# Optimization experiments

Measured on AMD Instinct MI355X. Metric: run time of the kernel, lower is better.

## Reference

```python
import jax, jax.numpy as jnp
import numpy as np

EPS = 1e-06


def _bilinear_sample(feat, coords_norm):
    """torch F.grid_sample(mode='bilinear', padding_mode='border', align_corners=False).
    feat: [B,C,H,W], coords_norm: [B,N,2] with (x,y) in [-1,1]. Returns [B,N,C]."""
    B, C, H, W = feat.shape
    # unnormalize (align_corners=False), then border-clip the coordinate
    x = jnp.clip(((coords_norm[..., 0] + 1.0) * W - 1.0) * 0.5, 0.0, W - 1.0)
    y = jnp.clip(((coords_norm[..., 1] + 1.0) * H - 1.0) * 0.5, 0.0, H - 1.0)
    x0 = jnp.floor(x); y0 = jnp.floor(y)
    wx = (x - x0)[:, None, :]; wy = (y - y0)[:, None, :]  # [B,1,N]
    x0i = x0.astype(jnp.int32); y0i = y0.astype(jnp.int32)
    x1i = jnp.minimum(x0i + 1, W - 1); y1i = jnp.minimum(y0i + 1, H - 1)
    flat = feat.reshape(B, C, H * W)
    def gather(yi, xi):
        idx = yi * W + xi  # [B,N]
        return jnp.take_along_axis(flat, idx[:, None, :], axis=2)  # [B,C,N]
    v00 = gather(y0i, x0i); v01 = gather(y0i, x1i)
    v10 = gather(y1i, x0i); v11 = gather(y1i, x1i)
    out = (v00 * (1 - wx) * (1 - wy) + v01 * wx * (1 - wy)
           + v10 * (1 - wx) * wy + v11 * wx * wy)
    return out.transpose(0, 2, 1)  # [B,N,C]


def _lin(x, w, b):
    return x @ w + b


def _forward(img, feat_s8, feat1_s8, feat_s16, ctx_s8, coarse_flow,
             ctx_w, ctx_b, gate1, ffn1_w1, ffn1_b1, ffn1_w2, ffn1_b2,
             s8_w, s8_b, gate2, ffn2_w1, ffn2_b1, ffn2_w2, ffn2_b2,
             hw1, hb1, hw2, hb2, hw3, hb3, hw4, hb4):
    B, _, H8, W8 = feat_s8.shape
    Hf, Wf = H8 * 8, W8 * 8
    # dense query grid in full-res pixel coords
    xs = jnp.arange(Wf, dtype=jnp.float32)
    ys = jnp.arange(Hf, dtype=jnp.float32)
    gx, gy = jnp.meshgrid(xs, ys)  # each [Hf,Wf]
    cn_x = jnp.clip(2.0 * (gx.reshape(-1) + 0.5) / Wf - 1.0, -1 + EPS, 1 - EPS)
    cn_y = jnp.clip(2.0 * (gy.reshape(-1) + 0.5) / Hf - 1.0, -1 + EPS, 1 - EPS)
    coords_norm = jnp.broadcast_to(jnp.stack([cn_x, cn_y], -1)[None], (B, Hf * Wf, 2))
    # five bilinear lookups
    f16 = _bilinear_sample(feat_s16, coords_norm)
    f8 = _bilinear_sample(feat_s8, coords_norm)
    fctx = _bilinear_sample(ctx_s8, coords_norm)
    # gated FFN fusion
    h2 = f8 + jax.nn.sigmoid(gate1) * _lin(fctx, ctx_w, ctx_b)
    h2 = _lin(jax.nn.gelu(_lin(h2, ffn1_w1, ffn1_b1), approximate=False), ffn1_w2, ffn1_b2)
    h3 = f16 + jax.nn.sigmoid(gate2) * _lin(h2, s8_w, s8_b)
    fused = _lin(jax.nn.gelu(_lin(h3, ffn2_w1, ffn2_b1), approximate=False), ffn2_w2, ffn2_b2)
    # coarse flow at queries, scaled to full-res pixels (Wf/W8 = Hf/H8 = 8)
    coarse = _bilinear_sample(coarse_flow, coords_norm) * jnp.array([Wf / W8, Hf / H8], jnp.float32)
    warp_x = coords_norm[..., 0] + 2.0 * coarse[..., 0] / Wf
    warp_y = coords_norm[..., 1] + 2.0 * coarse[..., 1] / Hf
    warped = jnp.clip(jnp.stack([warp_x, warp_y], -1), -1 + EPS, 1 - EPS)
    f1w = _bilinear_sample(feat1_s8, warped)
    coarse_norm = coarse / jnp.array([Wf, Hf], jnp.float32)
    mlp_in = jnp.concatenate([fused, f1w, coords_norm, coarse_norm], axis=-1)  # [B,N,260]
    h = jax.nn.relu(_lin(mlp_in, hw1, hb1))
    h = jax.nn.relu(_lin(h, hw2, hb2))
    h = jax.nn.relu(_lin(h, hw3, hb3))
    delta_norm = _lin(h, hw4, hb4)  # [B,N,2]
    flow = coarse + delta_norm * jnp.array([Wf, Hf], jnp.float32)
    return flow.reshape(B, Hf, Wf, 2).transpose(0, 3, 1, 2)


def setup_inputs() -> dict:
    key = jax.random.key(0)
    ks = jax.random.split(key, 24)
    hd = 128
    d = {
        'img': jax.random.normal(ks[0], (2, 3, 384, 512), jnp.float32),
        'feat_s8': jax.random.normal(ks[1], (2, 128, 48, 64), jnp.float32),
        'feat1_s8': jax.random.normal(ks[2], (2, 128, 48, 64), jnp.float32),
        'feat_s16': jax.random.normal(ks[3], (2, 128, 24, 32), jnp.float32),
        'ctx_s8': jax.random.normal(ks[4], (2, 64, 48, 64), jnp.float32),
        'coarse_flow': jax.random.normal(ks[5], (2, 2, 48, 64), jnp.float32),
        'ctx_w': jax.random.normal(ks[6], (64, hd), jnp.float32) * 0.05,
        'ctx_b': jnp.zeros((hd,), jnp.float32),
        'gate1': jnp.ones((hd,), jnp.float32),
        'ffn1_w1': jax.random.normal(ks[7], (hd, 2 * hd), jnp.float32) * 0.05,
        'ffn1_b1': jnp.zeros((2 * hd,), jnp.float32),
        'ffn1_w2': jax.random.normal(ks[8], (2 * hd, hd), jnp.float32) * 0.05,
        'ffn1_b2': jnp.zeros((hd,), jnp.float32),
        's8_w': jax.random.normal(ks[9], (hd, hd), jnp.float32) * 0.05,
        's8_b': jnp.zeros((hd,), jnp.float32),
        'gate2': jnp.ones((hd,), jnp.float32),
        'ffn2_w1': jax.random.normal(ks[10], (hd, 2 * hd), jnp.float32) * 0.05,
        'ffn2_b1': jnp.zeros((2 * hd,), jnp.float32),
        'ffn2_w2': jax.random.normal(ks[11], (2 * hd, hd), jnp.float32) * 0.05,
        'ffn2_b2': jnp.zeros((hd,), jnp.float32),
        'hw1': jax.random.normal(ks[12], (hd + 128 + 2 + 2, 256), jnp.float32) * 0.05,
        'hb1': jnp.zeros((256,), jnp.float32),
        'hw2': jax.random.normal(ks[13], (256, 128), jnp.float32) * 0.05,
        'hb2': jnp.zeros((128,), jnp.float32),
        'hw3': jax.random.normal(ks[14], (128, 64), jnp.float32) * 0.05,
        'hb3': jnp.zeros((64,), jnp.float32),
        'hw4': jax.random.normal(ks[15], (64, 2), jnp.float32) * 0.05,
        'hb4': jnp.zeros((2,), jnp.float32),
    }
    return d


def reference(img, feat_s8, feat1_s8, feat_s16, ctx_s8, coarse_flow,
              ctx_w, ctx_b, gate1, ffn1_w1, ffn1_b1, ffn1_w2, ffn1_b2,
              s8_w, s8_b, gate2, ffn2_w1, ffn2_b1, ffn2_w2, ffn2_b2,
              hw1, hb1, hw2, hb2, hw3, hb3, hw4, hb4):
    return _forward(img, feat_s8, feat1_s8, feat_s16, ctx_s8, coarse_flow,
                    ctx_w, ctx_b, gate1, ffn1_w1, ffn1_b1, ffn1_w2, ffn1_b2,
                    s8_w, s8_b, gate2, ffn2_w1, ffn2_b1, ffn2_w2, ffn2_b2,
                    hw1, hb1, hw2, hb2, hw3, hb3, hw4, hb4)
```

## Files before the change

### kernel.cpp

```cpp
#include <hip/hip_runtime.h>
#include <math.h>


typedef _Float16 half8 __attribute__((ext_vector_type(8)));
typedef _Float16 half4v __attribute__((ext_vector_type(4)));
typedef _Float16 half2v __attribute__((ext_vector_type(2)));
typedef float floatx4 __attribute__((ext_vector_type(4)));

#define NPOINTS_TOTAL (2 * 384 * 512)
#define PPB 64
#define NBLOCKS (NPOINTS_TOTAL / PPB)
#define PTS_PER_IMG 196608
#define BLOCKS_PER_IMG 3072

#define WS_CTX   0
#define WS_F1W1  8192
#define WS_F1W2  40960
#define WS_S8    73728
#define WS_F2W1  90112
#define WS_F2W2  122880
#define WS_HW1   155648
#define WS_HW2   221184
#define WS_HW3   253952

#define SB_CTXB  0
#define SB_GATE1 128
#define SB_F1B1  256
#define SB_F1B2  512
#define SB_S8B   640
#define SB_GATE2 768
#define SB_F2B1  896
#define SB_F2B2  1152
#define SB_HB1   1280
#define SB_HB2   1536
#define SB_HB3   1664
#define SB_TOT   1728

__device__ __forceinline__ float sigmoidf_(float x) { return 1.0f / (1.0f + expf(-x)); }
__device__ __forceinline__ float geluf_(float x) {
    const float ax = fabsf(x) * 0.70710678118654752f;
    const float t = 1.0f / fmaf(0.3275911f, ax, 1.0f);
    float poly = fmaf(t, 1.061405429f, -1.453152027f);
    poly = fmaf(t, poly, 1.421413741f);
    poly = fmaf(t, poly, -0.284496736f);
    poly = fmaf(t, poly, 0.254829592f);
    poly *= t;
    float er = 1.0f - poly * expf(-ax * ax);
    er = copysignf(er, x);
    return 0.5f * x * (1.0f + er);
}
__device__ __forceinline__ int swz(int pt) { return (pt & 15) << 3; }

__global__ void prepack_kernel(const float* __restrict__ ctx_w, const float* __restrict__ f1w1,
                               const float* __restrict__ f1w2, const float* __restrict__ s8w,
                               const float* __restrict__ f2w1, const float* __restrict__ f2w2,
                               const float* __restrict__ hw1, const float* __restrict__ hw2,
                               const float* __restrict__ hw3, _Float16* __restrict__ ws) {
    const int bid = blockIdx.x;
    const int lane = threadIdx.x;
    const float* src; int N, CT, start; size_t ofsH;
    if (bid < 16)       { src = ctx_w; N = 128; CT = 8;  start = 0;   ofsH = WS_CTX; }
    else if (bid < 80)  { src = f1w1;  N = 256; CT = 16; start = 16;  ofsH = WS_F1W1; }
    else if (bid < 144) { src = f1w2;  N = 128; CT = 8;  start = 80;  ofsH = WS_F1W2; }
    else if (bid < 176) { src = s8w;   N = 128; CT = 8;  start = 144; ofsH = WS_S8; }
    else if (bid < 240) { src = f2w1;  N = 256; CT = 16; start = 176; ofsH = WS_F2W1; }
    else if (bid < 304) { src = f2w2;  N = 128; CT = 8;  start = 240; ofsH = WS_F2W2; }
    else if (bid < 432) { src = hw1;   N = 256; CT = 16; start = 304; ofsH = WS_HW1; }
    else if (bid < 496) { src = hw2;   N = 128; CT = 8;  start = 432; ofsH = WS_HW2; }
    else                { src = hw3;   N = 64;  CT = 4;  start = 496; ofsH = WS_HW3; }
    const int ti = bid - start;
    const int ks = ti / CT, ct = ti % CT;
    const int m = lane & 15, g = lane >> 4;
    const int kb = ks * 32 + g * 8;
    const int n = ct * 16 + m;
    half8 v;
#pragma unroll
    for (int j = 0; j < 8; ++j) v[j] = (_Float16)src[(size_t)(kb + j) * N + n];
    *reinterpret_cast<half8*>(ws + ofsH + (size_t)ti * 512 + lane * 8) = v;
}

template <int NT, int CTc>
__device__ __forceinline__ void stageChunk(const _Float16* __restrict__ src, int cts,
                                           int ks0, int ct0, _Float16* wdst,
                                           int wid, int lane) {
#pragma unroll
    for (int jj = 0; jj < NT / 4; ++jj) {
        const int j = wid * (NT / 4) + jj;
        const int ks = j / CTc, ct = j - ks * CTc;
        const _Float16* s = src + (((size_t)(ks0 + ks) * cts + (ct0 + ct)) << 9) + lane * 8;
        _Float16* d = wdst + ((size_t)j << 9);
        __builtin_amdgcn_global_load_lds(
            (const __attribute__((address_space(1))) unsigned int*)s,
            (__attribute__((address_space(3))) unsigned int*)d, 16, 0, 0);
    }
}

template <int KSc, int CT>
__device__ __forceinline__ void gemmChunk(floatx4 (&acc)[CT], const _Float16* wlds,
                                          const _Float16* sact, int kbase, int ptb, int lane) {
    const int m = lane & 15, g = lane >> 4;
    const int pt0 = ptb + m;
    const int s0 = swz(pt0);
    const _Float16* wb = wlds + lane * 8;
    __builtin_amdgcn_s_setprio(1);
#pragma unroll
    for (int ks = 0; ks < KSc; ++ks) {
        half8 a = *reinterpret_cast<const half8*>(
            sact + pt0 * 128 + ((((kbase + ks) * 32) + g * 8) ^ s0));
        const _Float16* wk = wb + ((size_t)(ks * CT) << 9);
#pragma unroll
        for (int ct = 0; ct < CT; ++ct) {
            half8 w = *reinterpret_cast<const half8*>(wk + ((size_t)ct << 9));
            acc[ct] = __builtin_amdgcn_mfma_f32_16x16x32_f16(w, a, acc[ct], 0, 0, 0);
        }
    }
    __builtin_amdgcn_s_setprio(0);
}

template <int KSc, int CT>
__device__ __forceinline__ void gemmChunkRegB(floatx4 (&acc)[CT], const _Float16* wlds,
                                              const half8 (&fr)[4], int frbase, int lane) {
    const _Float16* wb = wlds + lane * 8;
    __builtin_amdgcn_s_setprio(1);
#pragma unroll
    for (int ks = 0; ks < KSc; ++ks) {
        const _Float16* wk = wb + ((size_t)(ks * CT) << 9);
#pragma unroll
        for (int ct = 0; ct < CT; ++ct) {
            half8 w = *reinterpret_cast<const half8*>(wk + ((size_t)ct << 9));
            acc[ct] = __builtin_amdgcn_mfma_f32_16x16x32_f16(w, fr[frbase + ks], acc[ct], 0, 0, 0);
        }
    }
    __builtin_amdgcn_s_setprio(0);
}

__device__ __forceinline__ void loadFrags(half8 (&fr)[4], const _Float16* sact, int ptb, int lane) {
    const int m = lane & 15, g = lane >> 4;
    const int pt0 = ptb + m;
    const int s0 = swz(pt0);
#pragma unroll
    for (int ks = 0; ks < 4; ++ks)
        fr[ks] = *reinterpret_cast<const half8*>(sact + pt0 * 128 + ((ks * 32 + g * 8) ^ s0));
}

__device__ __forceinline__ void storeH4(_Float16* dst, int pt, int ch0,
                                        float o0, float o1, float o2, float o3) {
    half4v hv;
    hv[0] = (_Float16)o0; hv[1] = (_Float16)o1; hv[2] = (_Float16)o2; hv[3] = (_Float16)o3;
    *reinterpret_cast<half4v*>(dst + pt * 128 + (ch0 ^ swz(pt))) = hv;
}
__device__ __forceinline__ half4v loadH4(const _Float16* src, int pt, int ch0) {
    return *reinterpret_cast<const half4v*>(src + pt * 128 + (ch0 ^ swz(pt)));
}

__global__ void __launch_bounds__(256, 2)
ifd_mfma(const float* __restrict__ feat_s8, const float* __restrict__ feat1_s8,
         const float* __restrict__ feat_s16, const float* __restrict__ ctx_s8,
         const float* __restrict__ coarse_flow,
         const float* __restrict__ ctx_b, const float* __restrict__ gate1,
         const float* __restrict__ ffn1_b1, const float* __restrict__ ffn1_b2,
         const float* __restrict__ s8_b, const float* __restrict__ gate2,
         const float* __restrict__ ffn2_b1, const float* __restrict__ ffn2_b2,
         const float* __restrict__ hw1, const float* __restrict__ hb1,
         const float* __restrict__ hb2, const float* __restrict__ hb3,
         const float* __restrict__ hw4, const float* __restrict__ hb4,
         const _Float16* __restrict__ wsp, float* __restrict__ out) {
    __shared__ __align__(16) _Float16 bufA[64 * 128];
    __shared__ __align__(16) _Float16 bufB[64 * 128];
    __shared__ __align__(16) _Float16 wBuf[2][8192];
    __shared__ __align__(16) float sBias[SB_TOT];
    __shared__ float sScal[4 * 64];
    __shared__ float sCps[2 * 64];
    __shared__ int   sIdx[3 * 4 * 64];
    __shared__ float sWgt[3 * 2 * 64];

    const int t = threadIdx.x;
    const int lane = t & 63, wid = t >> 6;
    const int m = lane & 15, g = lane >> 4;
    const int ptb = wid * 16;
    const int b = blockIdx.x / BLOCKS_PER_IMG;
    const int qbase = blockIdx.x * PPB;
    const float CHI = 1.0f - 1e-6f;

    if (t < 128) {
        sBias[SB_CTXB + t] = ctx_b[t];
        sBias[SB_GATE1 + t] = gate1[t];
        sBias[SB_F1B2 + t] = ffn1_b2[t];
        sBias[SB_S8B + t] = s8_b[t];
        sBias[SB_GATE2 + t] = gate2[t];
        sBias[SB_F2B2 + t] = ffn2_b2[t];
        sBias[SB_HB2 + t] = hb2[t];
    }
    sBias[SB_F1B1 + t] = ffn1_b1[t];
    sBias[SB_F2B1 + t] = ffn2_b1[t];
    sBias[SB_HB1 + t] = hb1[t];
    if (t < 64) sBias[SB_HB3 + t] = hb3[t];

    if (t < 64) {
        const int p = t;
        const int rem = qbase + p - b * PTS_PER_IMG;
        const int gy = rem >> 9, gx = rem & 511;
        float cnx = fminf(fmaxf(2.0f * ((float)gx + 0.5f) / 512.0f - 1.0f, -CHI), CHI);
        float cny = fminf(fmaxf(2.0f * ((float)gy + 0.5f) / 384.0f - 1.0f, -CHI), CHI);

        auto mkc = [](float cn, float Sf, int Smax, int& i0, int& i1, float& w) {
            float x = fminf(fmaxf(((cn + 1.0f) * Sf - 1.0f) * 0.5f, 0.0f), Sf - 1.0f);
            float xf = floorf(x);
            w = x - xf;
            i0 = (int)xf;
            i1 = (i0 + 1 > Smax) ? Smax : i0 + 1;
        };
        auto storeSet = [&](int s, int x0, int x1, int y0, int y1, float wx, float wy) {
            sIdx[s * 256 + 0 * 64 + p] = x0; sIdx[s * 256 + 1 * 64 + p] = x1;
            sIdx[s * 256 + 2 * 64 + p] = y0; sIdx[s * 256 + 3 * 64 + p] = y1;
            sWgt[s * 128 + p] = wx; sWgt[s * 128 + 64 + p] = wy;
        };

        int x0, x1, y0, y1; float wx, wy;
        mkc(cnx, 64.0f, 63, x0, x1, wx);
        mkc(cny, 48.0f, 47, y0, y1, wy);
        storeSet(0, x0, x1, y0, y1, wx, wy);

        int X0, X1, Y0, Y1; float WX, WY;
        mkc(cnx, 32.0f, 31, X0, X1, WX);
        mkc(cny, 24.0f, 23, Y0, Y1, WY);
        storeSet(1, X0, X1, Y0, Y1, WX, WY);

        const float w00 = (1.0f - wx) * (1.0f - wy), w01 = wx * (1.0f - wy);
        const float w10 = (1.0f - wx) * wy, w11 = wx * wy;
        const int i00 = y0 * 64 + x0, i01 = y0 * 64 + x1, i10 = y1 * 64 + x0, i11 = y1 * 64 + x1;
        const float* cf = coarse_flow + (size_t)b * 6144;
        float c0 = (cf[i00] * w00 + cf[i01] * w01 + cf[i10] * w10 + cf[i11] * w11) * 8.0f;
        const float* cf1 = cf + 3072;
        float c1 = (cf1[i00] * w00 + cf1[i01] * w01 + cf1[i10] * w10 + cf1[i11] * w11) * 8.0f;
        sCps[p] = c0; sCps[64 + p] = c1;
        sScal[p] = cnx; sScal[64 + p] = cny;
        sScal[128 + p] = c0 / 512.0f; sScal[192 + p] = c1 / 384.0f;

        float wxn = fminf(fmaxf(cnx + 2.0f * c0 / 512.0f, -CHI), CHI);
        float wyn = fminf(fmaxf(cny + 2.0f * c1 / 384.0f, -CHI), CHI);
        int u0, u1, v0, v1; float uw, vw;
        mkc(wxn, 64.0f, 63, u0, u1, uw);
        mkc(wyn, 48.0f, 47, v0, v1, vw);
        storeSet(2, u0, u1, v0, v1, uw, vw);
    }

    stageChunk<16, 8>(wsp + WS_CTX, 8, 0, 0, wBuf[0], wid, lane);
    __syncthreads();

    auto sampleMap = [&](const float* __restrict__ mapB, int C, int HW, int Wd, int set,
                         _Float16* dst) {
        const int pt = t & 63, hs = t >> 6;
        const int x0 = sIdx[set * 256 + pt], x1 = sIdx[set * 256 + 64 + pt];
        const int y0 = sIdx[set * 256 + 128 + pt], y1 = sIdx[set * 256 + 192 + pt];
        const float wx = sWgt[set * 128 + pt], wy = sWgt[set * 128 + 64 + pt];
        const float w00 = (1.0f - wx) * (1.0f - wy), w01 = wx * (1.0f - wy);
        const float w10 = (1.0f - wx) * wy, w11 = wx * wy;
        const int i00 = y0 * Wd + x0, i01 = y0 * Wd + x1, i10 = y1 * Wd + x0, i11 = y1 * Wd + x1;
        const int np = C >> 3;
#pragma unroll 4
        for (int i = 0; i < np; ++i) {
            const int c0 = hs * (C >> 2) + 2 * i;
            const float* p0 = mapB + (size_t)c0 * HW;
            const float* p1 = p0 + HW;
            float v0 = p0[i00] * w00 + p0[i01] * w01 + p0[i10] * w10 + p0[i11] * w11;
            float v1 = p1[i00] * w00 + p1[i01] * w01 + p1[i10] * w10 + p1[i11] * w11;
            half2v hv; hv[0] = (_Float16)v0; hv[1] = (_Float16)v1;
            *reinterpret_cast<half2v*>(dst + pt * 128 + (c0 ^ swz(pt))) = hv;
        }
    };

    sampleMap(feat_s8 + (size_t)b * 128 * 3072, 128, 3072, 64, 0, bufA);
    sampleMap(ctx_s8 + (size_t)b * 64 * 3072, 64, 3072, 64, 0, bufB);
    __syncthreads();

    const int pt = ptb + m;
    int cur = 0;
    floatx4 acc[8];

#define RESET8() do { _Pragma("unroll") for (int c = 0; c < 8; ++c) acc[c] = (floatx4)0.0f; } while (0)
#define STEP_END() do { __syncthreads(); cur ^= 1; } while (0)

    stageChunk<16, 8>(wsp + WS_F1W1, 16, 0, 0, wBuf[cur ^ 1], wid, lane);
    RESET8();
    gemmChunk<2, 8>(acc, wBuf[cur], bufB, 0, ptb, lane);
#pragma unroll
    for (int ct = 0; ct < 8; ++ct) {
        const int ch0 = ct * 16 + g * 4;
        const float4 bb = *reinterpret_cast<const float4*>(sBias + SB_CTXB + ch0);
        const float4 gg = *reinterpret_cast<const float4*>(sBias + SB_GATE1 + ch0);
        half4v rv = loadH4(bufA, pt, ch0);
        floatx4 v = acc[ct];
        storeH4(bufA, pt, ch0,
                (float)rv[0] + sigmoidf_(gg.x) * (v[0] + bb.x),
                (float)rv[1] + sigmoidf_(gg.y) * (v[1] + bb.y),
                (float)rv[2] + sigmoidf_(gg.z) * (v[2] + bb.z),
                (float)rv[3] + sigmoidf_(gg.w) * (v[3] + bb.w));
    }
    STEP_END();

    stageChunk<16, 8>(wsp + WS_F1W1, 16, 2, 0, wBuf[cur ^ 1], wid, lane);
    RESET8();
    gemmChunk<2, 8>(acc, wBuf[cur], bufA, 0, ptb, lane);
    STEP_END();
    stageChunk<16, 8>(wsp + WS_F1W1, 16, 0, 8, wBuf[cur ^ 1], wid, lane);
    gemmChunk<2, 8>(acc, wBuf[cur], bufA, 2, ptb, lane);
#pragma unroll
    for (int ct = 0; ct < 8; ++ct) {
        const int ch0 = ct * 16 + g * 4;
        const float4 bb = *reinterpret_cast<const float4*>(sBias + SB_F1B1 + ch0);
        floatx4 v = acc[ct];
        storeH4(bufB, pt, ch0, geluf_(v[0] + bb.x), geluf_(v[1] + bb.y),
                geluf_(v[2] + bb.z), geluf_(v[3] + bb.w));
    }
    STEP_END();

    stageChunk<16, 8>(wsp + WS_F1W1, 16, 2, 8, wBuf[cur ^ 1], wid, lane);
    RESET8();
    gemmChunk<2, 8>(acc, wBuf[cur], bufA, 0, ptb, lane);
    STEP_END();
    stageChunk<16, 8>(wsp + WS_F1W2, 8, 0, 0, wBuf[cur ^ 1], wid, lane);
    gemmChunk<2, 8>(acc, wBuf[cur], bufA, 2, ptb, lane);
#pragma unroll
    for (int ct = 0; ct < 8; ++ct) {
        const int ch0 = ct * 16 + g * 4;
        const float4 bb = *reinterpret_cast<const float4*>(sBias + SB_F1B1 + 128 + ch0);
        floatx4 v = acc[ct];
        storeH4(bufA, pt, ch0, geluf_(v[0] + bb.x), geluf_(v[1] + bb.y),
                geluf_(v[2] + bb.z), geluf_(v[3] + bb.w));
    }
    STEP_END();

    stageChunk<16, 8>(wsp + WS_F1W2, 8, 2, 0, wBuf[cur ^ 1], wid, lane);
    RESET8();
    gemmChunk<2, 8>(acc, wBuf[cur], bufB, 0, ptb, lane);
    STEP_END();
    stageChunk<16, 8>(wsp + WS_F1W2, 8, 4, 0, wBuf[cur ^ 1], wid, lane);
    gemmChunk<2, 8>(acc, wBuf[cur], bufB, 2, ptb, lane);
    STEP_END();
    stageChunk<16, 8>(wsp + WS_F1W2, 8, 6, 0, wBuf[cur ^ 1], wid, lane);
    gemmChunk<2, 8>(acc, wBuf[cur], bufA, 0, ptb, lane);
    STEP_END();
    stageChunk<16, 8>(wsp + WS_S8, 8, 0, 0, wBuf[cur ^ 1], wid, lane);
    gemmChunk<2, 8>(acc, wBuf[cur], bufA, 2, ptb, lane);
#pragma unroll
    for (int ct = 0; ct < 8; ++ct) {
        const int ch0 = ct * 16 + g * 4;
        const float4 bb = *reinterpret_cast<const float4*>(sBias + SB_F1B2 + ch0);
        floatx4 v = acc[ct];
        storeH4(bufA, pt, ch0, v[0] + bb.x, v[1] + bb.y, v[2] + bb.z, v[3] + bb.w);
    }
    STEP_END();

    sampleMap(feat_s16 + (size_t)b * 128 * 768, 128, 768, 32, 1, bufB);
    __syncthreads();

    stageChunk<16, 8>(wsp + WS_S8, 8, 2, 0, wBuf[cur ^ 1], wid, lane);
    RESET8();
    gemmChunk<2, 8>(acc, wBuf[cur], bufA, 0, ptb, lane);
    STEP_END();
    stageChunk<16, 8>(wsp + WS_F2W1, 16, 0, 0, wBuf[cur ^ 1], wid, lane);
    gemmChunk<2, 8>(acc, wBuf[cur], bufA, 2, ptb, lane);
#pragma unroll
    for (int ct = 0; ct < 8; ++ct) {
        const int ch0 = ct * 16 + g * 4;
        const float4 bb = *reinterpret_cast<const float4*>(sBias + SB_S8B + ch0);
        const float4 gg = *reinterpret_cast<const float4*>(sBias + SB_GATE2 + ch0);
        half4v rv = loadH4(bufB, pt, ch0);
        floatx4 v = acc[ct];
        storeH4(bufB, pt, ch0,
                (float)rv[0] + sigmoidf_(gg.x) * (v[0] + bb.x),
                (float)rv[1] + sigmoidf_(gg.y) * (v[1] + bb.y),
                (float)rv[2] + sigmoidf_(gg.z) * (v[2] + bb.z),
                (float)rv[3] + sigmoidf_(gg.w) * (v[3] + bb.w));
    }
    STEP_END();

    stageChunk<16, 8>(wsp + WS_F2W1, 16, 2, 0, wBuf[cur ^ 1], wid, lane);
    RESET8();
    gemmChunk<2, 8>(acc, wBuf[cur], bufB, 0, ptb, lane);
    STEP_END();
    stageChunk<16, 8>(wsp + WS_F2W1, 16, 0, 8, wBuf[cur ^ 1], wid, lane);
    gemmChunk<2, 8>(acc, wBuf[cur], bufB, 2, ptb, lane);
#pragma unroll
    for (int ct = 0; ct < 8; ++ct) {
        const int ch0 = ct * 16 + g * 4;
        const float4 bb = *reinterpret_cast<const float4*>(sBias + SB_F2B1 + ch0);
        floatx4 v = acc[ct];
        storeH4(bufA, pt, ch0, geluf_(v[0] + bb.x), geluf_(v[1] + bb.y),
                geluf_(v[2] + bb.z), geluf_(v[3] + bb.w));
    }
    STEP_END();

    stageChunk<16, 8>(wsp + WS_F2W1, 16, 2, 8, wBuf[cur ^ 1], wid, lane);
    RESET8();
    gemmChunk<2, 8>(acc, wBuf[cur], bufB, 0, ptb, lane);
    STEP_END();
    stageChunk<16, 8>(wsp + WS_F2W2, 8, 0, 0, wBuf[cur ^ 1], wid, lane);
    gemmChunk<2, 8>(acc, wBuf[cur], bufB, 2, ptb, lane);
#pragma unroll
    for (int ct = 0; ct < 8; ++ct) {
        const int ch0 = ct * 16 + g * 4;
        const float4 bb = *reinterpret_cast<const float4*>(sBias + SB_F2B1 + 128 + ch0);
        floatx4 v = acc[ct];
        storeH4(bufB, pt, ch0, geluf_(v[0] + bb.x), geluf_(v[1] + bb.y),
                geluf_(v[2] + bb.z), geluf_(v[3] + bb.w));
    }
    STEP_END();

    stageChunk<16, 8>(wsp + WS_F2W2, 8, 2, 0, wBuf[cur ^ 1], wid, lane);
    RESET8();
    gemmChunk<2, 8>(acc, wBuf[cur], bufA, 0, ptb, lane);
    STEP_END();
    stageChunk<16, 8>(wsp + WS_F2W2, 8, 4, 0, wBuf[cur ^ 1], wid, lane);
    gemmChunk<2, 8>(acc, wBuf[cur], bufA, 2, ptb, lane);
    STEP_END();
    stageChunk<16, 8>(wsp + WS_F2W2, 8, 6, 0, wBuf[cur ^ 1], wid, lane);
    gemmChunk<2, 8>(acc, wBuf[cur], bufB, 0, ptb, lane);
    STEP_END();
    stageChunk<16, 8>(wsp + WS_HW1, 16, 0, 0, wBuf[cur ^ 1], wid, lane);
    gemmChunk<2, 8>(acc, wBuf[cur], bufB, 2, ptb, lane);
#pragma unroll
    for (int ct = 0; ct < 8; ++ct) {
        const int ch0 = ct * 16 + g * 4;
        const float4 bb = *reinterpret_cast<const float4*>(sBias + SB_F2B2 + ch0);
        floatx4 v = acc[ct];
        storeH4(bufB, pt, ch0, v[0] + bb.x, v[1] + bb.y, v[2] + bb.z, v[3] + bb.w);
    }
    STEP_END();

    sampleMap(feat1_s8 + (size_t)b * 128 * 3072, 128, 3072, 64, 2, bufA);
    __syncthreads();

    half8 fr[4];
    loadFrags(fr, bufA, ptb, lane);
    stageChunk<16, 8>(wsp + WS_HW1, 16, 2, 0, wBuf[cur ^ 1], wid, lane);
    RESET8();
    gemmChunk<2, 8>(acc, wBuf[cur], bufB, 0, ptb, lane);
    STEP_END();
    stageChunk<16, 8>(wsp + WS_HW1, 16, 4, 0, wBuf[cur ^ 1], wid, lane);
    gemmChunk<2, 8>(acc, wBuf[cur], bufB, 2, ptb, lane);
    STEP_END();
    stageChunk<16, 8>(wsp + WS_HW1, 16, 6, 0, wBuf[cur ^ 1], wid, lane);
    gemmChunkRegB<2, 8>(acc, wBuf[cur], fr, 0, lane);
    STEP_END();
    stageChunk<16, 8>(wsp + WS_HW1, 16, 0, 8, wBuf[cur ^ 1], wid, lane);
    gemmChunkRegB<2, 8>(acc, wBuf[cur], fr, 2, lane);
#pragma unroll
    for (int ct = 0; ct < 8; ++ct) {
        const int ch0 = ct * 16 + g * 4;
#pragma unroll
        for (int jj = 0; jj < 4; ++jj) {
            const float4 wj = *reinterpret_cast<const float4*>(hw1 + (size_t)(256 + jj) * 256 + ch0);
            const float s = sScal[jj * 64 + pt];
            floatx4 v = acc[ct];
            v[0] = fmaf(wj.x, s, v[0]); v[1] = fmaf(wj.y, s, v[1]);
            v[2] = fmaf(wj.z, s, v[2]); v[3] = fmaf(wj.w, s, v[3]);
            acc[ct] = v;
        }
        const float4 bb = *reinterpret_cast<const float4*>(sBias + SB_HB1 + ch0);
        floatx4 v = acc[ct];
        storeH4(bufA, pt, ch0, fmaxf(v[0] + bb.x, 0.0f), fmaxf(v[1] + bb.y, 0.0f),
                fmaxf(v[2] + bb.z, 0.0f), fmaxf(v[3] + bb.w, 0.0f));
    }
    STEP_END();

    stageChunk<16, 8>(wsp + WS_HW1, 16, 2, 8, wBuf[cur ^ 1], wid, lane);
    RESET8();
    gemmChunk<2, 8>(acc, wBuf[cur], bufB, 0, ptb, lane);
    STEP_END();
    stageChunk<16, 8>(wsp + WS_HW1, 16, 4, 8, wBuf[cur ^ 1], wid, lane);
    gemmChunk<2, 8>(acc, wBuf[cur], bufB, 2, ptb, lane);
    STEP_END();
    stageChunk<16, 8>(wsp + WS_HW1, 16, 6, 8, wBuf[cur ^ 1], wid, lane);
    gemmChunkRegB<2, 8>(acc, wBuf[cur], fr, 0, lane);
    STEP_END();
    stageChunk<16, 8>(wsp + WS_HW2, 8, 0, 0, wBuf[cur ^ 1], wid, lane);
    gemmChunkRegB<2, 8>(acc, wBuf[cur], fr, 2, lane);
#pragma unroll
    for (int ct = 0; ct < 8; ++ct) {
        const int ch0 = ct * 16 + g * 4;
#pragma unroll
        for (int jj = 0; jj < 4; ++jj) {
            const float4 wj = *reinterpret_cast<const float4*>(hw1 + (size_t)(256 + jj) * 256 + 128 + ch0);
            const float s = sScal[jj * 64 + pt];
            floatx4 v = acc[ct];
            v[0] = fmaf(wj.x, s, v[0]); v[1] = fmaf(wj.y, s, v[1]);
            v[2] = fmaf(wj.z, s, v[2]); v[3] = fmaf(wj.w, s, v[3]);
            acc[ct] = v;
        }
        const float4 bb = *reinterpret_cast<const float4*>(sBias + SB_HB1 + 128 + ch0);
        floatx4 v = acc[ct];
        storeH4(bufB, pt, ch0, fmaxf(v[0] + bb.x, 0.0f), fmaxf(v[1] + bb.y, 0.0f),
                fmaxf(v[2] + bb.z, 0.0f), fmaxf(v[3] + bb.w, 0.0f));
    }
    STEP_END();

    stageChunk<16, 8>(wsp + WS_HW2, 8, 2, 0, wBuf[cur ^ 1], wid, lane);
    RESET8();
    gemmChunk<2, 8>(acc, wBuf[cur], bufA, 0, ptb, lane);
    STEP_END();
    stageChunk<16, 8>(wsp + WS_HW2, 8, 4, 0, wBuf[cur ^ 1], wid, lane);
    gemmChunk<2, 8>(acc, wBuf[cur], bufA, 2, ptb, lane);
    STEP_END();
    stageChunk<16, 8>(wsp + WS_HW2, 8, 6, 0, wBuf[cur ^ 1], wid, lane);
    gemmChunk<2, 8>(acc, wBuf[cur], bufB, 0, ptb, lane);
    STEP_END();
    stageChunk<16, 4>(wsp + WS_HW3, 4, 0, 0, wBuf[cur ^ 1], wid, lane);
    gemmChunk<2, 8>(acc, wBuf[cur], bufB, 2, ptb, lane);
#pragma unroll
    for (int ct = 0; ct < 8; ++ct) {
        const int ch0 = ct * 16 + g * 4;
        const float4 bb = *reinterpret_cast<const float4*>(sBias + SB_HB2 + ch0);
        floatx4 v = acc[ct];
        storeH4(bufA, pt, ch0, fmaxf(v[0] + bb.x, 0.0f), fmaxf(v[1] + bb.y, 0.0f),
                fmaxf(v[2] + bb.z, 0.0f), fmaxf(v[3] + bb.w, 0.0f));
    }
    STEP_END();

    {
        floatx4 acc4[4];
#pragma unroll
        for (int c = 0; c < 4; ++c) acc4[c] = (floatx4)0.0f;
        gemmChunk<4, 4>(acc4, wBuf[cur], bufA, 0, ptb, lane);
#pragma unroll
        for (int ct = 0; ct < 4; ++ct) {
            const int ch0 = ct * 16 + g * 4;
            const float4 bb = *reinterpret_cast<const float4*>(sBias + SB_HB3 + ch0);
            floatx4 v = acc4[ct];
            storeH4(bufB, pt, ch0, fmaxf(v[0] + bb.x, 0.0f), fmaxf(v[1] + bb.y, 0.0f),
                    fmaxf(v[2] + bb.z, 0.0f), fmaxf(v[3] + bb.w, 0.0f));
        }
    }
    __syncthreads();

    if (t < 128) {
        const int pp = t >> 1, j = t & 1;
        float d = hb4[j];
#pragma unroll
        for (int i8 = 0; i8 < 8; ++i8) {
            const int c0 = i8 * 8;
            half8 hv = *reinterpret_cast<const half8*>(bufB + pp * 128 + (c0 ^ swz(pp)));
#pragma unroll
            for (int j2 = 0; j2 < 8; ++j2)
                d = fmaf((float)hv[j2], hw4[(c0 + j2) * 2 + j], d);
        }
        const int q = qbase + pp;
        const int rem = q - b * PTS_PER_IMG;
        const int gy = rem >> 9, gx = rem & 511;
        const float flow = sCps[j * 64 + pp] + d * (j == 0 ? 512.0f : 384.0f);
        out[(((size_t)b * 2 + j) * 384 + gy) * 512 + gx] = flow;
    }
#undef RESET8
#undef STEP_END
}

extern "C" void kernel_launch(void* const* d_in, const int* in_sizes, int n_in,
                              void* d_out, int out_size, void* d_ws, size_t ws_size,
                              hipStream_t stream) {
    const float* feat_s8 = (const float*)d_in[1];
    const float* feat1_s8 = (const float*)d_in[2];
    const float* feat_s16 = (const float*)d_in[3];
    const float* ctx_s8 = (const float*)d_in[4];
    const float* coarse_flow = (const float*)d_in[5];
    const float* ctx_w = (const float*)d_in[6];
    const float* ctx_b = (const float*)d_in[7];
    const float* gate1 = (const float*)d_in[8];
    const float* ffn1_w1 = (const float*)d_in[9];
    const float* ffn1_b1 = (const float*)d_in[10];
    const float* ffn1_w2 = (const float*)d_in[11];
    const float* ffn1_b2 = (const float*)d_in[12];
    const float* s8_w = (const float*)d_in[13];
    const float* s8_b = (const float*)d_in[14];
    const float* gate2 = (const float*)d_in[15];
    const float* ffn2_w1 = (const float*)d_in[16];
    const float* ffn2_b1 = (const float*)d_in[17];
    const float* ffn2_w2 = (const float*)d_in[18];
    const float* ffn2_b2 = (const float*)d_in[19];
    const float* hw1 = (const float*)d_in[20];
    const float* hb1 = (const float*)d_in[21];
    const float* hw2 = (const float*)d_in[22];
    const float* hb2 = (const float*)d_in[23];
    const float* hw3 = (const float*)d_in[24];
    const float* hb3 = (const float*)d_in[25];
    const float* hw4 = (const float*)d_in[26];
    const float* hb4 = (const float*)d_in[27];
    float* out = (float*)d_out;
    _Float16* wsp = (_Float16*)d_ws;

    prepack_kernel<<<dim3(512), dim3(64), 0, stream>>>(
        ctx_w, ffn1_w1, ffn1_w2, s8_w, ffn2_w1, ffn2_w2, hw1, hw2, hw3, wsp);

    ifd_mfma<<<dim3(NBLOCKS), dim3(256), 0, stream>>>(
        feat_s8, feat1_s8, feat_s16, ctx_s8, coarse_flow,
        ctx_b, gate1, ffn1_b1, ffn1_b2, s8_b, gate2, ffn2_b1, ffn2_b2,
        hw1, hb1, hb2, hb3, hw4, hb4, wsp, out);
}
```

Baseline: 702.0 us.

## Retile MFMA GEMMs so each wave computes 32 points by 4 channel tiles

Changes the per-wave work split in every fused MLP GEMM. Instead of each wave owning 16 points across all 8 output channel tiles, waves now own 32 points across 4 channel tiles. Each weight fragment read from LDS therefore feeds two MFMAs, halving weight LDS traffic per MFMA at the cost of twice as many activation reads. Because waves now write output channels that other waves read in place, extra __syncthreads are added before epilogues that overwrite an input buffer, which adds barrier cost.

After: 629.9 us, median of 2. 1.11x faster.

```diff
diff --git a/kernel.cpp b/kernel.cpp
--- a/kernel.cpp
+++ b/kernel.cpp
@@ -95,52 +95,81 @@
     }
 }
 
-template <int KSc, int CT>
-__device__ __forceinline__ void gemmChunk(floatx4 (&acc)[CT], const _Float16* wlds,
-                                          const _Float16* sact, int kbase, int ptb, int lane) {
+template <int KSc>
+__device__ __forceinline__ void gemmChunkQ(floatx4 (&acc)[4][2], const _Float16* wlds,
+                                           const _Float16* sact, int kbase,
+                                           int ctb, int ptb, int lane) {
     const int m = lane & 15, g = lane >> 4;
-    const int pt0 = ptb + m;
-    const int s0 = swz(pt0);
+    const int pt0 = ptb + m, pt1 = pt0 + 16;
+    const int s0 = swz(pt0), s1 = swz(pt1);
     const _Float16* wb = wlds + lane * 8;
     __builtin_amdgcn_s_setprio(1);
 #pragma unroll
     for (int ks = 0; ks < KSc; ++ks) {
-        half8 a = *reinterpret_cast<const half8*>(
-            sact + pt0 * 128 + ((((kbase + ks) * 32) + g * 8) ^ s0));
-        const _Float16* wk = wb + ((size_t)(ks * CT) << 9);
-#pragma unroll
-        for (int ct = 0; ct < CT; ++ct) {
-            half8 w = *reinterpret_cast<const half8*>(wk + ((size_t)ct << 9));
-            acc[ct] = __builtin_amdgcn_mfma_f32_16x16x32_f16(w, a, acc[ct], 0, 0, 0);
+        const int k0 = (kbase + ks) * 32 + g * 8;
+        half8 a0 = *reinterpret_cast<const half8*>(sact + pt0 * 128 + (k0 ^ s0));
+        half8 a1 = *reinterpret_cast<const half8*>(sact + pt1 * 128 + (k0 ^ s1));
+#pragma unroll
+        for (int c = 0; c < 4; ++c) {
+            half8 w = *reinterpret_cast<const half8*>(wb + ((size_t)(ks * 8 + ctb + c) << 9));
+            acc[c][0] = __builtin_amdgcn_mfma_f32_16x16x32_f16(w, a0, acc[c][0], 0, 0, 0);
+            acc[c][1] = __builtin_amdgcn_mfma_f32_16x16x32_f16(w, a1, acc[c][1], 0, 0, 0);
         }
     }
     __builtin_amdgcn_s_setprio(0);
 }
 
-template <int KSc, int CT>
-__device__ __forceinline__ void gemmChunkRegB(floatx4 (&acc)[CT], const _Float16* wlds,
-                                              const half8 (&fr)[4], int frbase, int lane) {
+template <int KSc>
+__device__ __forceinline__ void gemmChunkRegBQ(floatx4 (&acc)[4][2], const _Float16* wlds,
+                                               const half8 (&fr)[4][2], int frbase,
+                                               int ctb, int lane) {
     const _Float16* wb = wlds + lane * 8;
     __builtin_amdgcn_s_setprio(1);
 #pragma unroll
     for (int ks = 0; ks < KSc; ++ks) {
-        const _Float16* wk = wb + ((size_t)(ks * CT) << 9);
-#pragma unroll
-        for (int ct = 0; ct < CT; ++ct) {
-            half8 w = *reinterpret_cast<const half8*>(wk + ((size_t)ct << 9));
-            acc[ct] = __builtin_amdgcn_mfma_f32_16x16x32_f16(w, fr[frbase + ks], acc[ct], 0, 0, 0);
+#pragma unroll
+        for (int c = 0; c < 4; ++c) {
+            half8 w = *reinterpret_cast<const half8*>(wb + ((size_t)(ks * 8 + ctb + c) << 9));
+            acc[c][0] = __builtin_amdgcn_mfma_f32_16x16x32_f16(w, fr[frbase + ks][0], acc[c][0], 0, 0, 0);
+            acc[c][1] = __builtin_amdgcn_mfma_f32_16x16x32_f16(w, fr[frbase + ks][1], acc[c][1], 0, 0, 0);
         }
     }
     __builtin_amdgcn_s_setprio(0);
 }
 
-__device__ __forceinline__ void loadFrags(half8 (&fr)[4], const _Float16* sact, int ptb, int lane) {
+__device__ __forceinline__ void gemmChunkH3(floatx4 (&acc)[2][2], const _Float16* wlds,
+                                            const _Float16* sact, int ctb2, int ptb, int lane) {
     const int m = lane & 15, g = lane >> 4;
-    const int pt0 = ptb + m;
-    const int s0 = swz(pt0);
-#pragma unroll
-    for (int ks = 0; ks < 4; ++ks)
-        fr[ks] = *reinterpret_cast<const half8*>(sact + pt0 * 128 + ((ks * 32 + g * 8) ^ s0));
+    const int pt0 = ptb + m, pt1 = pt0 + 16;
+    const int s0 = swz(pt0), s1 = swz(pt1);
+    const _Float16* wb = wlds + lane * 8;
+    __builtin_amdgcn_s_setprio(1);
+#pragma unroll
+    for (int ks = 0; ks < 4; ++ks) {
+        const int k0 = ks * 32 + g * 8;
+        half8 a0 = *reinterpret_cast<const half8*>(sact + pt0 * 128 + (k0 ^ s0));
+        half8 a1 = *reinterpret_cast<const half8*>(sact + pt1 * 128 + (k0 ^ s1));
+#pragma unroll
+        for (int c = 0; c < 2; ++c) {
+            half8 w = *reinterpret_cast<const half8*>(wb + ((size_t)(ks * 4 + ctb2 + c) << 9));
+            acc[c][0] = __builtin_amdgcn_mfma_f32_16x16x32_f16(w, a0, acc[c][0], 0, 0, 0);
+            acc[c][1] = __builtin_amdgcn_mfma_f32_16x16x32_f16(w, a1, acc[c][1], 0, 0, 0);
+        }
+    }
+    __builtin_amdgcn_s_setprio(0);
+}
+
+__device__ __forceinline__ void loadFragsQ(half8 (&fr)[4][2], const _Float16* sact,
+                                           int ptb, int lane) {
+    const int m = lane & 15, g = lane >> 4;
+    const int pt0 = ptb + m, pt1 = pt0 + 16;
+    const int s0 = swz(pt0), s1 = swz(pt1);
+#pragma unroll
+    for (int ks = 0; ks < 4; ++ks) {
+        const int k0 = ks * 32 + g * 8;
+        fr[ks][0] = *reinterpret_cast<const half8*>(sact + pt0 * 128 + (k0 ^ s0));
+        fr[ks][1] = *reinterpret_cast<const half8*>(sact + pt1 * 128 + (k0 ^ s1));
+    }
 }
 
 __device__ __forceinline__ void storeH4(_Float16* dst, int pt, int ch0,
@@ -177,7 +206,8 @@
     const int t = threadIdx.x;
     const int lane = t & 63, wid = t >> 6;
     const int m = lane & 15, g = lane >> 4;
-    const int ptb = wid * 16;
+    const int ctb = (wid & 1) * 4;
+    const int ptb = (wid >> 1) * 32;
     const int b = blockIdx.x / BLOCKS_PER_IMG;
     const int qbase = blockIdx.x * PPB;
     const float CHI = 1.0f - 1e-6f;
@@ -274,262 +304,261 @@
     sampleMap(ctx_s8 + (size_t)b * 64 * 3072, 64, 3072, 64, 0, bufB);
     __syncthreads();
 
-    const int pt = ptb + m;
     int cur = 0;
-    floatx4 acc[8];
-
-#define RESET8() do { _Pragma("unroll") for (int c = 0; c < 8; ++c) acc[c] = (floatx4)0.0f; } while (0)
+    floatx4 acc[4][2];
+
+#define RESETQ() do { _Pragma("unroll") for (int _c = 0; _c < 4; ++_c) \
+    { acc[_c][0] = (floatx4)0.0f; acc[_c][1] = (floatx4)0.0f; } } while (0)
 #define STEP_END() do { __syncthreads(); cur ^= 1; } while (0)
 
+#define EPI_LOOP(BODY) do { \
+    _Pragma("unroll") for (int c = 0; c < 4; ++c) { \
+        const int ch0 = (ctb + c) * 16 + g * 4; \
+        _Pragma("unroll") for (int pg = 0; pg < 2; ++pg) { \
+            const int pt2 = ptb + pg * 16 + m; \
+            floatx4 v = acc[c][pg]; \
+            BODY \
+        } } } while (0)
+
     stageChunk<16, 8>(wsp + WS_F1W1, 16, 0, 0, wBuf[cur ^ 1], wid, lane);
-    RESET8();
-    gemmChunk<2, 8>(acc, wBuf[cur], bufB, 0, ptb, lane);
-#pragma unroll
-    for (int ct = 0; ct < 8; ++ct) {
-        const int ch0 = ct * 16 + g * 4;
+    RESETQ();
+    gemmChunkQ<2>(acc, wBuf[cur], bufB, 0, ctb, ptb, lane);
+    EPI_LOOP({
         const float4 bb = *reinterpret_cast<const float4*>(sBias + SB_CTXB + ch0);
         const float4 gg = *reinterpret_cast<const float4*>(sBias + SB_GATE1 + ch0);
-        half4v rv = loadH4(bufA, pt, ch0);
-        floatx4 v = acc[ct];
-        storeH4(bufA, pt, ch0,
+        half4v rv = loadH4(bufA, pt2, ch0);
+        storeH4(bufA, pt2, ch0,
                 (float)rv[0] + sigmoidf_(gg.x) * (v[0] + bb.x),
                 (float)rv[1] + sigmoidf_(gg.y) * (v[1] + bb.y),
                 (float)rv[2] + sigmoidf_(gg.z) * (v[2] + bb.z),
                 (float)rv[3] + sigmoidf_(gg.w) * (v[3] + bb.w));
-    }
+    });
     STEP_END();
 
     stageChunk<16, 8>(wsp + WS_F1W1, 16, 2, 0, wBuf[cur ^ 1], wid, lane);
-    RESET8();
-    gemmChunk<2, 8>(acc, wBuf[cur], bufA, 0, ptb, lane);
+    RESETQ();
+    gemmChunkQ<2>(acc, wBuf[cur], bufA, 0, ctb, ptb, lane);
     STEP_END();
     stageChunk<16, 8>(wsp + WS_F1W1, 16, 0, 8, wBuf[cur ^ 1], wid, lane);
-    gemmChunk<2, 8>(acc, wBuf[cur], bufA, 2, ptb, lane);
-#pragma unroll
-    for (int ct = 0; ct < 8; ++ct) {
-        const int ch0 = ct * 16 + g * 4;
+    gemmChunkQ<2>(acc, wBuf[cur], bufA, 2, ctb, ptb, lane);
+    EPI_LOOP({
         const float4 bb = *reinterpret_cast<const float4*>(sBias + SB_F1B1 + ch0);
-        floatx4 v = acc[ct];
-        storeH4(bufB, pt, ch0, geluf_(v[0] + bb.x), geluf_(v[1] + bb.y),
+        storeH4(bufB, pt2, ch0, geluf_(v[0] + bb.x), geluf_(v[1] + bb.y),
                 geluf_(v[2] + bb.z), geluf_(v[3] + bb.w));
-    }
+    });
     STEP_END();
 
     stageChunk<16, 8>(wsp + WS_F1W1, 16, 2, 8, wBuf[cur ^ 1], wid, lane);
-    RESET8();
-    gemmChunk<2, 8>(acc, wBuf[cur], bufA, 0, ptb, lane);
+    RESETQ();
+    gemmChunkQ<2>(acc, wBuf[cur], bufA, 0, ctb, ptb, lane);
     STEP_END();
     stageChunk<16, 8>(wsp + WS_F1W2, 8, 0, 0, wBuf[cur ^ 1], wid, lane);
-    gemmChunk<2, 8>(acc, wBuf[cur], bufA, 2, ptb, lane);
-#pragma unroll
-    for (int ct = 0; ct < 8; ++ct) {
-        const int ch0 = ct * 16 + g * 4;
+    gemmChunkQ<2>(acc, wBuf[cur], bufA, 2, ctb, ptb, lane);
+    __syncthreads();
+    EPI_LOOP({
         const float4 bb = *reinterpret_cast<const float4*>(sBias + SB_F1B1 + 128 + ch0);
-        floatx4 v = acc[ct];
-        storeH4(bufA, pt, ch0, geluf_(v[0] + bb.x), geluf_(v[1] + bb.y),
+        storeH4(bufA, pt2, ch0, geluf_(v[0] + bb.x), geluf_(v[1] + bb.y),
                 geluf_(v[2] + bb.z), geluf_(v[3] + bb.w));
-    }
+    });
     STEP_END();
 
     stageChunk<16, 8>(wsp + WS_F1W2, 8, 2, 0, wBuf[cur ^ 1], wid, lane);
-    RESET8();
-    gemmChunk<2, 8>(acc, wBuf[cur], bufB, 0, ptb, lane);
+    RESETQ();
+    gemmChunkQ<2>(acc, wBuf[cur], bufB, 0, ctb, ptb, lane);
     STEP_END();
     stageChunk<16, 8>(wsp + WS_F1W2, 8, 4, 0, wBuf[cur ^ 1], wid, lane);
-    gemmChunk<2, 8>(acc, wBuf[cur], bufB, 2, ptb, lane);
+    gemmChunkQ<2>(acc, wBuf[cur], bufB, 2, ctb, ptb, lane);
     STEP_END();
     stageChunk<16, 8>(wsp + WS_F1W2, 8, 6, 0, wBuf[cur ^ 1], wid, lane);
-    gemmChunk<2, 8>(acc, wBuf[cur], bufA, 0, ptb, lane);
+    gemmChunkQ<2>(acc, wBuf[cur], bufA, 0, ctb, ptb, lane);
     STEP_END();
     stageChunk<16, 8>(wsp + WS_S8, 8, 0, 0, wBuf[cur ^ 1], wid, lane);
-    gemmChunk<2, 8>(acc, wBuf[cur], bufA, 2, ptb, lane);
-#pragma unroll
-    for (int ct = 0; ct < 8; ++ct) {
-        const int ch0 = ct * 16 + g * 4;
+    gemmChunkQ<2>(acc, wBuf[cur], bufA, 2, ctb, ptb, lane);
+    __syncthreads();
+    EPI_LOOP({
         const float4 bb = *reinterpret_cast<const float4*>(sBias + SB_F1B2 + ch0);
-        floatx4 v = acc[ct];
-        storeH4(bufA, pt, ch0, v[0] + bb.x, v[1] + bb.y, v[2] + bb.z, v[3] + bb.w);
-    }
+        storeH4(bufA, pt2, ch0, v[0] + bb.x, v[1] + bb.y, v[2] + bb.z, v[3] + bb.w);
+    });
     STEP_END();
 
     sampleMap(feat_s16 + (size_t)b * 128 * 768, 128, 768, 32, 1, bufB);
     __syncthreads();
 
     stageChunk<16, 8>(wsp + WS_S8, 8, 2, 0, wBuf[cur ^ 1], wid, lane);
-    RESET8();
-    gemmChunk<2, 8>(acc, wBuf[cur], bufA, 0, ptb, lane);
+    RESETQ();
+    gemmChunkQ<2>(acc, wBuf[cur], bufA, 0, ctb, ptb, lane);
     STEP_END();
     stageChunk<16, 8>(wsp + WS_F2W1, 16, 0, 0, wBuf[cur ^ 1], wid, lane);
-    gemmChunk<2, 8>(acc, wBuf[cur], bufA, 2, ptb, lane);
-#pragma unroll
-    for (int ct = 0; ct < 8; ++ct) {
-        const int ch0 = ct * 16 + g * 4;
+    gemmChunkQ<2>(acc, wBuf[cur], bufA, 2, ctb, ptb, lane);
+    EPI_LOOP({
         const float4 bb = *reinterpret_cast<const float4*>(sBias + SB_S8B + ch0);
         const float4 gg = *reinterpret_cast<const float4*>(sBias + SB_GATE2 + ch0);
-        half4v rv = loadH4(bufB, pt, ch0);
-        floatx4 v = acc[ct];
-        storeH4(bufB, pt, ch0,
+        half4v rv = loadH4(bufB, pt2, ch0);
+        storeH4(bufB, pt2, ch0,
                 (float)rv[0] + sigmoidf_(gg.x) * (v[0] + bb.x),
                 (float)rv[1] + sigmoidf_(gg.y) * (v[1] + bb.y),
                 (float)rv[2] + sigmoidf_(gg.z) * (v[2] + bb.z),
                 (float)rv[3] + sigmoidf_(gg.w) * (v[3] + bb.w));
-    }
+    });
     STEP_END();
 
     stageChunk<16, 8>(wsp + WS_F2W1, 16, 2, 0, wBuf[cur ^ 1], wid, lane);
-    RESET8();
-    gemmChunk<2, 8>(acc, wBuf[cur], bufB, 0, ptb, lane);
+    RESETQ();
+    gemmChunkQ<2>(acc, wBuf[cur], bufB, 0, ctb, ptb, lane);
     STEP_END();
     stageChunk<16, 8>(wsp + WS_F2W1, 16, 0, 8, wBuf[cur ^ 1], wid, lane);
-    gemmChunk<2, 8>(acc, wBuf[cur], bufB, 2, ptb, lane);
-#pragma unroll
-    for (int ct = 0; ct < 8; ++ct) {
-        const int ch0 = ct * 16 + g * 4;
+    gemmChunkQ<2>(acc, wBuf[cur], bufB, 2, ctb, ptb, lane);
+    EPI_LOOP({
         const float4 bb = *reinterpret_cast<const float4*>(sBias + SB_F2B1 + ch0);
-        floatx4 v = acc[ct];
-        storeH4(bufA, pt, ch0, geluf_(v[0] + bb.x), geluf_(v[1] + bb.y),
+        storeH4(bufA, pt2, ch0, geluf_(v[0] + bb.x), geluf_(v[1] + bb.y),
                 geluf_(v[2] + bb.z), geluf_(v[3] + bb.w));
-    }
+    });
     STEP_END();
 
     stageChunk<16, 8>(wsp + WS_F2W1, 16, 2, 8, wBuf[cur ^ 1], wid, lane);
-    RESET8();
-    gemmChunk<2, 8>(acc, wBuf[cur], bufB, 0, ptb, lane);
+    RESETQ();
+    gemmChunkQ<2>(acc, wBuf[cur], bufB, 0, ctb, ptb, lane);
     STEP_END();
     stageChunk<16, 8>(wsp + WS_F2W2, 8, 0, 0, wBuf[cur ^ 1], wid, lane);
-    gemmChunk<2, 8>(acc, wBuf[cur], bufB, 2, ptb, lane);
-#pragma unroll
-    for (int ct = 0; ct < 8; ++ct) {
-        const int ch0 = ct * 16 + g * 4;
+    gemmChunkQ<2>(acc, wBuf[cur], bufB, 2, ctb, ptb, lane);
+    __syncthreads();
+    EPI_LOOP({
         const float4 bb = *reinterpret_cast<const float4*>(sBias + SB_F2B1 + 128 + ch0);
-        floatx4 v = acc[ct];
-        storeH4(bufB, pt, ch0, geluf_(v[0] + bb.x), geluf_(v[1] + bb.y),
+        storeH4(bufB, pt2, ch0, geluf_(v[0] + bb.x), geluf_(v[1] + bb.y),
                 geluf_(v[2] + bb.z), geluf_(v[3] + bb.w));
-    }
+    });
     STEP_END();
 
     stageChunk<16, 8>(wsp + WS_F2W2, 8, 2, 0, wBuf[cur ^ 1], wid, lane);
-    RESET8();
-    gemmChunk<2, 8>(acc, wBuf[cur], bufA, 0, ptb, lane);
+    RESETQ();
+    gemmChunkQ<2>(acc, wBuf[cur], bufA, 0, ctb, ptb, lane);
     STEP_END();
     stageChunk<16, 8>(wsp + WS_F2W2, 8, 4, 0, wBuf[cur ^ 1], wid, lane);
-    gemmChunk<2, 8>(acc, wBuf[cur], bufA, 2, ptb, lane);
+    gemmChunkQ<2>(acc, wBuf[cur], bufA, 2, ctb, ptb, lane);
     STEP_END();
     stageChunk<16, 8>(wsp + WS_F2W2, 8, 6, 0, wBuf[cur ^ 1], wid, lane);
-    gemmChunk<2, 8>(acc, wBuf[cur], bufB, 0, ptb, lane);
+    gemmChunkQ<2>(acc, wBuf[cur], bufB, 0, ctb, ptb, lane);
     STEP_END();
     stageChunk<16, 8>(wsp + WS_HW1, 16, 0, 0, wBuf[cur ^ 1], wid, lane);
-    gemmChunk<2, 8>(acc, wBuf[cur], bufB, 2, ptb, lane);
-#pragma unroll
-    for (int ct = 0; ct < 8; ++ct) {
-        const int ch0 = ct * 16 + g * 4;
+    gemmChunkQ<2>(acc, wBuf[cur], bufB, 2, ctb, ptb, lane);
+    __syncthreads();
+    EPI_LOOP({
         const float4 bb = *reinterpret_cast<const float4*>(sBias + SB_F2B2 + ch0);
-        floatx4 v = acc[ct];
-        storeH4(bufB, pt, ch0, v[0] + bb.x, v[1] + bb.y, v[2] + bb.z, v[3] + bb.w);
-    }
+        storeH4(bufB, pt2, ch0, v[0] + bb.x, v[1] + bb.y, v[2] + bb.z, v[3] + bb.w);
+    });
     STEP_END();
 
     sampleMap(feat1_s8 + (size_t)b * 128 * 3072, 128, 3072, 64, 2, bufA);
     __syncthreads();
 
-    half8 fr[4];
-    loadFrags(fr, bufA, ptb, lane);
+    half8 fr[4][2];
+    loadFragsQ(fr, bufA, ptb, lane);
     stageChunk<16, 8>(wsp + WS_HW1, 16, 2, 0, wBuf[cur ^ 1], wid, lane);
-    RESET8();
-    gemmChunk<2, 8>(acc, wBuf[cur], bufB, 0, ptb, lane);
+    RESETQ();
+    gemmChunkQ<2>(acc, wBuf[cur], bufB, 0, ctb, ptb, lane);
     STEP_END();
     stageChunk<16, 8>(wsp + WS_HW1, 16, 4, 0, wBuf[cur ^ 1], wid, lane);
-    gemmChunk<2, 8>(acc, wBuf[cur], bufB, 2, ptb, lane);
+    gemmChunkQ<2>(acc, wBuf[cur], bufB, 2, ctb, ptb, lane);
     STEP_END();
     stageChunk<16, 8>(wsp + WS_HW1, 16, 6, 0, wBuf[cur ^ 1], wid, lane);
-    gemmChunkRegB<2, 8>(acc, wBuf[cur], fr, 0, lane);
+    gemmChunkRegBQ<2>(acc, wBuf[cur], fr, 0, ctb, lane);
     STEP_END();
     stageChunk<16, 8>(wsp + WS_HW1, 16, 0, 8, wBuf[cur ^ 1], wid, lane);
-    gemmChunkRegB<2, 8>(acc, wBuf[cur], fr, 2, lane);
-#pragma unroll
-    for (int ct = 0; ct < 8; ++ct) {
-        const int ch0 = ct * 16 + g * 4;
+    gemmChunkRegBQ<2>(acc, wBuf[cur], fr, 2, ctb, lane);
+#pragma unroll
+    for (int c = 0; c < 4; ++c) {
+        const int ch0 = (ctb + c) * 16 + g * 4;
 #pragma unroll
         for (int jj = 0; jj < 4; ++jj) {
             const float4 wj = *reinterpret_cast<const float4*>(hw1 + (size_t)(256 + jj) * 256 + ch0);
-            const float s = sScal[jj * 64 + pt];
-            floatx4 v = acc[ct];
-            v[0] = fmaf(wj.x, s, v[0]); v[1] = fmaf(wj.y, s, v[1]);
-            v[2] = fmaf(wj.z, s, v[2]); v[3] = fmaf(wj.w, s, v[3]);
-            acc[ct] = v;
-        }
+#pragma unroll
+            for (int pg = 0; pg < 2; ++pg) {
+                const float s = sScal[jj * 64 + ptb + pg * 16 + m];
+                floatx4 v = acc[c][pg];
+                v[0] = fmaf(wj.x, s, v[0]); v[1] = fmaf(wj.y, s, v[1]);
+                v[2] = fmaf(wj.z, s, v[2]); v[3] = fmaf(wj.w, s, v[3]);
+                acc[c][pg] = v;
+            }
+        }
+    }
+    EPI_LOOP({
         const float4 bb = *reinterpret_cast<const float4*>(sBias + SB_HB1 + ch0);
-        floatx4 v = acc[ct];
-        storeH4(bufA, pt, ch0, fmaxf(v[0] + bb.x, 0.0f), fmaxf(v[1] + bb.y, 0.0f),
+        storeH4(bufA, pt2, ch0, fmaxf(v[0] + bb.x, 0.0f), fmaxf(v[1] + bb.y, 0.0f),
                 fmaxf(v[2] + bb.z, 0.0f), fmaxf(v[3] + bb.w, 0.0f));
-    }
+    });
     STEP_END();
 
     stageChunk<16, 8>(wsp + WS_HW1, 16, 2, 8, wBuf[cur ^ 1], wid, lane);
-    RESET8();
-    gemmChunk<2, 8>(acc, wBuf[cur], bufB, 0, ptb, lane);
+    RESETQ();
+    gemmChunkQ<2>(acc, wBuf[cur], bufB, 0, ctb, ptb, lane);
     STEP_END();
     stageChunk<16, 8>(wsp + WS_HW1, 16, 4, 8, wBuf[cur ^ 1], wid, lane);
-    gemmChunk<2, 8>(acc, wBuf[cur], bufB, 2, ptb, lane);
+    gemmChunkQ<2>(acc, wBuf[cur], bufB, 2, ctb, ptb, lane);
     STEP_END();
     stageChunk<16, 8>(wsp + WS_HW1, 16, 6, 8, wBuf[cur ^ 1], wid, lane);
-    gemmChunkRegB<2, 8>(acc, wBuf[cur], fr, 0, lane);
+    gemmChunkRegBQ<2>(acc, wBuf[cur], fr, 0, ctb, lane);
     STEP_END();
     stageChunk<16, 8>(wsp + WS_HW2, 8, 0, 0, wBuf[cur ^ 1], wid, lane);
-    gemmChunkRegB<2, 8>(acc, wBuf[cur], fr, 2, lane);
-#pragma unroll
-    for (int ct = 0; ct < 8; ++ct) {
-        const int ch0 = ct * 16 + g * 4;
+    gemmChunkRegBQ<2>(acc, wBuf[cur], fr, 2, ctb, lane);
+#pragma unroll
+    for (int c = 0; c < 4; ++c) {
+        const int ch0 = (ctb + c) * 16 + g * 4;
 #pragma unroll
         for (int jj = 0; jj < 4; ++jj) {
             const float4 wj = *reinterpret_cast<const float4*>(hw1 + (size_t)(256 + jj) * 256 + 128 + ch0);
-            const float s = sScal[jj * 64 + pt];
-            floatx4 v = acc[ct];
-            v[0] = fmaf(wj.x, s, v[0]); v[1] = fmaf(wj.y, s, v[1]);
-            v[2] = fmaf(wj.z, s, v[2]); v[3] = fmaf(wj.w, s, v[3]);
-            acc[ct] = v;
-        }
+#pragma unroll
+            for (int pg = 0; pg < 2; ++pg) {
+                const float s = sScal[jj * 64 + ptb + pg * 16 + m];
+                floatx4 v = acc[c][pg];
+                v[0] = fmaf(wj.x, s, v[0]); v[1] = fmaf(wj.y, s, v[1]);
+                v[2] = fmaf(wj.z, s, v[2]); v[3] = fmaf(wj.w, s, v[3]);
+                acc[c][pg] = v;
+            }
+        }
+    }
+    EPI_LOOP({
         const float4 bb = *reinterpret_cast<const float4*>(sBias + SB_HB1 + 128 + ch0);
-        floatx4 v = acc[ct];
-        storeH4(bufB, pt, ch0, fmaxf(v[0] + bb.x, 0.0f), fmaxf(v[1] + bb.y, 0.0f),
+        storeH4(bufB, pt2, ch0, fmaxf(v[0] + bb.x, 0.0f), fmaxf(v[1] + bb.y, 0.0f),
                 fmaxf(v[2] + bb.z, 0.0f), fmaxf(v[3] + bb.w, 0.0f));
-    }
+    });
     STEP_END();
 
     stageChunk<16, 8>(wsp + WS_HW2, 8, 2, 0, wBuf[cur ^ 1], wid, lane);
-    RESET8();
-    gemmChunk<2, 8>(acc, wBuf[cur], bufA, 0, ptb, lane);
+    RESETQ();
+    gemmChunkQ<2>(acc, wBuf[cur], bufA, 0, ctb, ptb, lane);
     STEP_END();
     stageChunk<16, 8>(wsp + WS_HW2, 8, 4, 0, wBuf[cur ^ 1], wid, lane);
-    gemmChunk<2, 8>(acc, wBuf[cur], bufA, 2, ptb, lane);
+    gemmChunkQ<2>(acc, wBuf[cur], bufA, 2, ctb, ptb, lane);
     STEP_END();
     stageChunk<16, 8>(wsp + WS_HW2, 8, 6, 0, wBuf[cur ^ 1], wid, lane);
-    gemmChunk<2, 8>(acc, wBuf[cur], bufB, 0, ptb, lane);
+    gemmChunkQ<2>(acc, wBuf[cur], bufB, 0, ctb, ptb, lane);
     STEP_END();
     stageChunk<16, 4>(wsp + WS_HW3, 4, 0, 0, wBuf[cur ^ 1], wid, lane);
-    gemmChunk<2, 8>(acc, wBuf[cur], bufB, 2, ptb, lane);
-#pragma unroll
-    for (int ct = 0; ct < 8; ++ct) {
-        const int ch0 = ct * 16 + g * 4;
+    gemmChunkQ<2>(acc, wBuf[cur], bufB, 2, ctb, ptb, lane);
+    EPI_LOOP({
         const float4 bb = *reinterpret_cast<const float4*>(sBias + SB_HB2 + ch0);
-        floatx4 v = acc[ct];
-        storeH4(bufA, pt, ch0, fmaxf(v[0] + bb.x, 0.0f), fmaxf(v[1] + bb.y, 0.0f),
+        storeH4(bufA, pt2, ch0, fmaxf(v[0] + bb.x, 0.0f), fmaxf(v[1] + bb.y, 0.0f),
                 fmaxf(v[2] + bb.z, 0.0f), fmaxf(v[3] + bb.w, 0.0f));
-    }
+    });
     STEP_END();
 
     {
-        floatx4 acc4[4];
-#pragma unroll
-        for (int c = 0; c < 4; ++c) acc4[c] = (floatx4)0.0f;
-        gemmChunk<4, 4>(acc4, wBuf[cur], bufA, 0, ptb, lane);
-#pragma unroll
-        for (int ct = 0; ct < 4; ++ct) {
-            const int ch0 = ct * 16 + g * 4;
+        const int ctb2 = (wid & 1) * 2;
+        floatx4 a3[2][2];
+#pragma unroll
+        for (int c = 0; c < 2; ++c) { a3[c][0] = (floatx4)0.0f; a3[c][1] = (floatx4)0.0f; }
+        gemmChunkH3(a3, wBuf[cur], bufA, ctb2, ptb, lane);
+#pragma unroll
+        for (int c = 0; c < 2; ++c) {
+            const int ch0 = (ctb2 + c) * 16 + g * 4;
             const float4 bb = *reinterpret_cast<const float4*>(sBias + SB_HB3 + ch0);
-            floatx4 v = acc4[ct];
-            storeH4(bufB, pt, ch0, fmaxf(v[0] + bb.x, 0.0f), fmaxf(v[1] + bb.y, 0.0f),
-                    fmaxf(v[2] + bb.z, 0.0f), fmaxf(v[3] + bb.w, 0.0f));
+#pragma unroll
+            for (int pg = 0; pg < 2; ++pg) {
+                const int pt2 = ptb + pg * 16 + m;
+                floatx4 v = a3[c][pg];
+                storeH4(bufB, pt2, ch0, fmaxf(v[0] + bb.x, 0.0f), fmaxf(v[1] + bb.y, 0.0f),
+                        fmaxf(v[2] + bb.z, 0.0f), fmaxf(v[3] + bb.w, 0.0f));
+            }
         }
     }
     __syncthreads();
@@ -551,8 +580,9 @@
         const float flow = sCps[j * 64 + pp] + d * (j == 0 ? 512.0f : 384.0f);
         out[(((size_t)b * 2 + j) * 384 + gy) * 512 + gx] = flow;
     }
-#undef RESET8
+#undef RESETQ
 #undef STEP_END
+#undef EPI_LOOP
 }
 
 extern "C" void kernel_launch(void* const* d_in, const int* in_sizes, int n_in,
```
